# Performance work log

Measured on AMD Instinct MI355X. Metric: run time of the kernel, lower is better.

Reference implementation:

```python
import jax, jax.numpy as jnp
import numpy as np

DIM, HEADS, WS = 256, 16, 8
B, H, W = 2, 252, 252
BN_EPS = 1e-5


def _rel_index():
    # Same construction as the torch buffer relative_position_index (64,64)
    coords = np.stack(np.meshgrid(np.arange(WS), np.arange(WS), indexing='ij'))
    flat = coords.reshape(2, -1)
    rel = (flat[:, :, None] - flat[:, None, :]).transpose(1, 2, 0).copy()
    rel[..., 0] += WS - 1
    rel[..., 1] += WS - 1
    rel[..., 0] *= 2 * WS - 1
    return jnp.asarray(rel.sum(-1))

REL_IDX = _rel_index()  # (WS*WS, WS*WS) int


def _conv(x, w, pad, groups=1):
    return jax.lax.conv_general_dilated(
        x, w, (1, 1), [(pad[0], pad[0]), (pad[1], pad[1])],
        dimension_numbers=('NCHW', 'OIHW', 'NCHW'), feature_group_count=groups)


def setup_inputs() -> dict:
    key = jax.random.key(0)
    ks = jax.random.split(key, 8)
    s = lambda k, shape, sc: jax.random.normal(k, shape, jnp.float32) * sc
    z = lambda: jnp.zeros((DIM,), jnp.float32)
    return {
        'x': s(ks[0], (B, DIM, H, W), 1.0),
        'w_qkv': s(ks[1], (3 * DIM, DIM, 1, 1), 0.05),
        'rel_bias_table': s(ks[2], ((2 * WS - 1) ** 2, HEADS), 0.02),
        'w_h': s(ks[3], (DIM, DIM, WS, 1), 0.02),
        'b_h': z(),
        'w_v': s(ks[4], (DIM, DIM, 1, WS), 0.02),
        'b_v': z(),
        'w_dw': s(ks[5], (DIM, 1, WS, WS), 0.05),
        'bn_gamma': jnp.ones((DIM,), jnp.float32),
        'bn_beta': z(),
        'bn_mean': z(),
        'bn_var': jnp.ones((DIM,), jnp.float32),
        'w_pw': s(ks[6], (DIM, DIM, 1, 1), 0.05),
    }


def reference(x, w_qkv, rel_bias_table, w_h, b_h, w_v, b_v, w_dw,
              bn_gamma, bn_beta, bn_mean, bn_var, w_pw):
    Bc, C, Hc, Wc = x.shape
    pad_h, pad_w = WS - Hc % WS, WS - Wc % WS
    xp = jnp.pad(x, ((0, 0), (0, 0), (0, pad_h), (0, pad_w)), mode='reflect')
    Hp, Wp = Hc + pad_h, Wc + pad_w
    hh, ww, d = Hp // WS, Wp // WS, C // HEADS

    qkv = _conv(xp, w_qkv, (0, 0))  # (B, 3C, Hp, Wp)
    # b (qkv h d) (hh ws1) (ww ws2) -> qkv (b hh ww) h (ws1 ws2) d
    qkv = qkv.reshape(Bc, 3, HEADS, d, hh, WS, ww, WS)
    qkv = qkv.transpose(1, 0, 4, 6, 2, 5, 7, 3).reshape(3, Bc * hh * ww, HEADS, WS * WS, d)
    q, k, v = qkv[0], qkv[1], qkv[2]

    dots = jnp.einsum('nhid,nhjd->nhij', q, k) * (d ** -0.5)
    bias = rel_bias_table[REL_IDX.reshape(-1)].reshape(WS * WS, WS * WS, HEADS)
    dots = dots + bias.transpose(2, 0, 1)[None]  # (1, h, 64, 64)
    attn = jax.nn.softmax(dots, axis=-1)
    out = jnp.einsum('nhij,nhjd->nhid', attn, v)
    # (b hh ww) h (ws1 ws2) d -> b (h d) (hh ws1) (ww ws2)
    out = out.reshape(Bc, hh, ww, HEADS, WS, WS, d)
    out = out.transpose(0, 3, 6, 1, 4, 2, 5).reshape(Bc, C, Hp, Wp)
    out = out[:, :, :Hc, :Wc]

    p1 = _conv(jnp.pad(out, ((0, 0), (0, 0), (0, 1), (0, 0)), mode='reflect'),
               w_h, (WS // 2 - 1, 0)) + b_h[None, :, None, None]
    p2 = _conv(jnp.pad(out, ((0, 0), (0, 0), (0, 0), (0, 1)), mode='reflect'),
               w_v, (0, WS // 2 - 1)) + b_v[None, :, None, None]
    y = jnp.pad(p1 + p2, ((0, 0), (0, 0), (0, 1), (0, 1)), mode='reflect')
    y = _conv(y, w_dw, ((WS - 1) // 2, (WS - 1) // 2), groups=DIM)  # depthwise
    inv = bn_gamma / jnp.sqrt(bn_var + BN_EPS)
    y = y * inv[None, :, None, None] + (bn_beta - bn_mean * inv)[None, :, None, None]
    y = _conv(y, w_pw, (0, 0))  # pointwise 1x1
    return y[:, :, :Hc, :Wc]
```

## Files before the change

kernel.cpp:

```cpp
#include <hip/hip_runtime.h>
#include <hip/hip_bf16.h>

#define HC 252
#define WC 252
#define CD 256
#define NHEADS 16

#define XP_W 264
#define XP_ROW (XP_W*256)
#define XP_BH  (252*XP_ROW)

typedef unsigned short u16;
typedef unsigned int u32;
typedef __attribute__((ext_vector_type(8))) short bf16x8;
typedef __attribute__((ext_vector_type(4))) float f32x4;
typedef __attribute__((ext_vector_type(4))) u32 u32x4;
typedef __attribute__((ext_vector_type(2))) u32 u32x2;

#define XP_BYTES (2u * 2u * (unsigned)XP_BH)
#define ZP_OFF   XP_BYTES
#define ZP_BYTES 409600u
#define WT_OFF   (ZP_OFF + ZP_BYTES)
#define WT_ELEMS (128*8192)
#define WPW_OFF  (WT_OFF + (unsigned)WT_ELEMS*2u)
#define WPW_ELEMS (8*8192)
#define WQ_OFF   (WPW_OFF + (unsigned)WPW_ELEMS*2u)
#define WQ_ELEMS (768*256)
#define BIAS_OFF (WQ_OFF + (unsigned)WQ_ELEMS*2u)
#define HALO_ZERO_ELEMS (2*252*11*256)

__device__ __forceinline__ u16 bfu(float f) {
    __hip_bfloat16 h = __float2bfloat16(f);
    return *(reinterpret_cast<u16*>(&h));
}
__device__ __forceinline__ u32 pack2(float a, float b) {
    return (u32)bfu(a) | ((u32)bfu(b) << 16);
}
__device__ __forceinline__ float bf2f(u16 v) {
    union { u32 u; float f; } cv; cv.u = ((u32)v) << 16; return cv.f;
}

__global__ __launch_bounds__(256, 2) void attn_mfma(
    const float* __restrict__ x, const u16* __restrict__ WQ,
    const float* __restrict__ BIASF, u16* __restrict__ xp)
{
    __shared__ __align__(16) char smem[57344];

    const int bid = blockIdx.x;
    const int zz = (bid & 7) * 256 + (bid >> 3);
    const int wx = zz & 31, wy = (zz >> 5) & 31, b = zz >> 10;
    const int tid = threadIdx.x;
    const int lane = tid & 63, wid = tid >> 6;
    const int g = lane >> 4, li = lane & 15;

    {
        int ci = tid;
        const float* srcc = x + (size_t)(b * 256 + ci) * (HC * WC);
        #pragma unroll
        for (int r = 0; r < 8; ++r) {
            int h = wy * 8 + r; if (h >= HC) h = 2 * HC - 2 - h;
            const float* src = srcc + h * WC;
            float v[8];
            if (wx == 31) {
                #pragma unroll
                for (int c = 0; c < 8; ++c) {
                    int w = 248 + c; if (w >= WC) w = 2 * WC - 2 - w;
                    v[c] = src[w];
                }
            } else {
                float4 f0 = *(const float4*)(src + wx * 8);
                float4 f1 = *(const float4*)(src + wx * 8 + 4);
                v[0]=f0.x; v[1]=f0.y; v[2]=f0.z; v[3]=f0.w;
                v[4]=f1.x; v[5]=f1.y; v[6]=f1.z; v[7]=f1.w;
            }
            #pragma unroll
            for (int c = 0; c < 8; ++c) {
                int pos = r * 8 + c;
                int byte = pos * 512 + ((ci * 2) ^ ((pos & 7) << 4));
                *(u16*)(smem + byte) = bfu(v[c]);
            }
        }
    }
    __syncthreads();

    const int WB = 32768 + wid * 6144;
    char* Vb = smem + WB;
    char* Pb = smem + WB + 2048;

    const bf16x8 zf = {0,0,0,0,0,0,0,0};

    #pragma unroll 1
    for (int hh = 0; hh < 4; ++hh) {
        const int head = wid * 4 + hh;

        f32x4 acc[3][4];
        #pragma unroll
        for (int p = 0; p < 3; ++p)
            #pragma unroll
            for (int nf = 0; nf < 4; ++nf) acc[p][nf] = (f32x4){0.f,0.f,0.f,0.f};

        for (int ks = 0; ks < 8; ++ks) {
            bf16x8 bx[4];
            #pragma unroll
            for (int nf = 0; nf < 4; ++nf) {
                int pos = 16 * nf + li;
                int byte = pos * 512 + ((ks * 64 + 16 * g) ^ ((pos & 7) << 4));
                bx[nf] = *(const bf16x8*)(smem + byte);
            }
            bf16x8 aw[3];
            #pragma unroll
            for (int p = 0; p < 3; ++p) {
                int o = p * 256 + head * 16 + li;
                aw[p] = *(const bf16x8*)(WQ + o * 256 + ks * 32 + 8 * g);
            }
            __builtin_amdgcn_s_setprio(1);
            #pragma unroll
            for (int p = 0; p < 3; ++p)
                #pragma unroll
                for (int nf = 0; nf < 4; ++nf)
                    acc[p][nf] = __builtin_amdgcn_mfma_f32_16x16x32_bf16(aw[p], bx[nf], acc[p][nf], 0, 0, 0);
            __builtin_amdgcn_s_setprio(0);
        }

        bf16x8 qf[4], kf[4];
        const int sA = 32 * g + li;
        #pragma unroll
        for (int nf = 0; nf < 4; ++nf) {
            #pragma unroll
            for (int p = 0; p < 2; ++p) {
                u32 w0 = pack2(acc[p][nf][0], acc[p][nf][1]);
                u32 w1 = pack2(acc[p][nf][2], acc[p][nf][3]);
                union { bf16x8 v; u32 u[4]; } f;
                f.u[0] = (u32)__shfl((int)w0, sA);
                f.u[1] = (u32)__shfl((int)w1, sA);
                f.u[2] = (u32)__shfl((int)w0, sA + 16);
                f.u[3] = (u32)__shfl((int)w1, sA + 16);
                bf16x8 fv = (g < 2) ? f.v : zf;
                if (p == 0) qf[nf] = fv; else kf[nf] = fv;
            }
        }

        #pragma unroll
        for (int nf = 0; nf < 4; ++nf) {
            int pos = 16 * nf + li;
            #pragma unroll
            for (int r = 0; r < 4; ++r) {
                int d = 4 * g + r;
                int byte = (pos >> 3) * 256 + d * 16 + (pos & 7) * 2;
                *(u16*)(Vb + byte) = bfu(acc[2][nf][r]);
            }
        }

        f32x4 s[4][4];
        #pragma unroll
        for (int mf = 0; mf < 4; ++mf)
            #pragma unroll
            for (int nf = 0; nf < 4; ++nf) s[mf][nf] = (f32x4){0.f,0.f,0.f,0.f};
        __builtin_amdgcn_s_setprio(1);
        #pragma unroll
        for (int mf = 0; mf < 4; ++mf)
            #pragma unroll
            for (int nf = 0; nf < 4; ++nf)
                s[mf][nf] = __builtin_amdgcn_mfma_f32_16x16x32_bf16(qf[mf], kf[nf], s[mf][nf], 0, 0, 0);
        __builtin_amdgcn_s_setprio(0);

        f32x4 e[4][4];
        f32x4 rs[4];
        #pragma unroll
        for (int mf = 0; mf < 4; ++mf) rs[mf] = (f32x4){0.f,0.f,0.f,0.f};
        #pragma unroll
        for (int mf = 0; mf < 4; ++mf)
            #pragma unroll
            for (int nf = 0; nf < 4; ++nf) {
                f32x4 b4 = *(const f32x4*)(BIASF + (((head * 4 + mf) * 4 + nf) * 64 + lane) * 4);
                #pragma unroll
                for (int r = 0; r < 4; ++r) {
                    float ev = __expf(s[mf][nf][r] * 0.25f + b4[r]);
                    e[mf][nf][r] = ev;
                    rs[mf][r] += ev;
                }
            }
        #pragma unroll
        for (int mf = 0; mf < 4; ++mf)
            #pragma unroll
            for (int r = 0; r < 4; ++r) {
                float t = rs[mf][r];
                t += __shfl_xor(t, 1); t += __shfl_xor(t, 2);
                t += __shfl_xor(t, 4); t += __shfl_xor(t, 8);
                rs[mf][r] = t;
            }

        f32x4 o[4];
        #pragma unroll
        for (int mf = 0; mf < 4; ++mf) o[mf] = (f32x4){0.f,0.f,0.f,0.f};
        const bool even = !(lane & 1);
        #pragma unroll
        for (int hf = 0; hf < 2; ++hf) {
            #pragma unroll
            for (int mf = 0; mf < 4; ++mf)
                #pragma unroll
                for (int nfl = 0; nfl < 2; ++nfl) {
                    f32x4 ee = e[mf][2 * hf + nfl];
                    float p0 = __shfl_xor(ee[0], 1), p1 = __shfl_xor(ee[1], 1);
                    float p2 = __shfl_xor(ee[2], 1), p3 = __shfl_xor(ee[3], 1);
                    int jl = 16 * nfl + (li & ~1);
                    u32 w0, w1; int r0;
                    if (even) { w0 = pack2(ee[0], p0); w1 = pack2(ee[1], p1); r0 = 0; }
                    else      { w0 = pack2(p2, ee[2]); w1 = pack2(p3, ee[3]); r0 = 2; }
                    int i0 = 16 * mf + 4 * g + r0, i1 = i0 + 1;
                    *(u32*)(Pb + i0 * 64 + ((2 * jl) ^ ((i0 & 3) << 4))) = w0;
                    *(u32*)(Pb + i1 * 64 + ((2 * jl) ^ ((i1 & 3) << 4))) = w1;
                }
            bf16x8 bv = *(const bf16x8*)(Vb + (4 * hf + g) * 256 + li * 16);
            __builtin_amdgcn_s_setprio(1);
            #pragma unroll
            for (int mf = 0; mf < 4; ++mf) {
                int i = 16 * mf + li;
                bf16x8 ap = *(const bf16x8*)(Pb + i * 64 + ((16 * g) ^ ((i & 3) << 4)));
                o[mf] = __builtin_amdgcn_mfma_f32_16x16x32_bf16(ap, bv, o[mf], 0, 0, 0);
            }
            __builtin_amdgcn_s_setprio(0);
        }

        #pragma unroll
        for (int mf = 0; mf < 4; ++mf) {
            int h = wy * 8 + 2 * mf + (g >> 1);
            int wbase = wx * 8 + 4 * (g & 1);
            if (h < HC && wbase < WC) {
                size_t rowb = ((size_t)(b * HC + h)) * XP_ROW + (size_t)(head * 16 + li);
                #pragma unroll
                for (int r = 0; r < 4; ++r) {
                    float v = o[mf][r] / rs[mf][r];
                    u16 bv = bfu(v);
                    xp[rowb + (size_t)(wbase + r + 4) * 256] = bv;
                    if (wbase + r == 250) xp[rowb + (size_t)256 * 256] = bv;
                }
            }
        }
    }
}

__global__ __launch_bounds__(256) void wprep_kernel(
    const float* __restrict__ wh, const float* __restrict__ wv,
    const float* __restrict__ wpw, const float* __restrict__ wqkv,
    const float* __restrict__ btab, u16* __restrict__ wsu)
{
    int i = blockIdx.x * 256 + threadIdx.x;
    u16* WT = wsu + WT_OFF / 2;
    u16* WP = wsu + WPW_OFF / 2;
    u16* ZP = wsu + ZP_OFF / 2;
    u16* WQp = wsu + WQ_OFF / 2;
    float* BF = (float*)(wsu + BIAS_OFF / 2);
    if (i < WT_ELEMS) {
        int j = i & 7, l = (i >> 3) & 1023, s = i >> 13;
        int kb = (l >> 8) & 3;
        int co = (l & 255) ^ (kb << 1);
        float v;
        if (s < 64) {
            int t = s >> 3, ci = (s & 7) * 32 + kb * 8 + j;
            v = wh[co * 2048 + ci * 8 + t];
        } else {
            int s2 = s - 64;
            int t = s2 >> 3, ci = (s2 & 7) * 32 + kb * 8 + j;
            v = wv[co * 2048 + ci * 8 + t];
        }
        WT[i] = bfu(v);
    } else if (i < WT_ELEMS + WPW_ELEMS) {
        int i2 = i - WT_ELEMS;
        int j = i2 & 7, l = (i2 >> 3) & 1023, s = i2 >> 13;
        int kb = (l >> 8) & 3;
        int co = (l & 255) ^ (kb << 1);
        WP[i2] = bfu(wpw[co * 256 + s * 32 + kb * 8 + j]);
    } else if (i < WT_ELEMS + WPW_ELEMS + (int)(ZP_BYTES / 2)) {
        ZP[i - WT_ELEMS - WPW_ELEMS] = 0;
    } else if (i < WT_ELEMS + WPW_ELEMS + (int)(ZP_BYTES / 2) + WQ_ELEMS) {
        int i4 = i - WT_ELEMS - WPW_ELEMS - (int)(ZP_BYTES / 2);
        WQp[i4] = bfu(wqkv[i4]);
    } else {
        int i5 = i - WT_ELEMS - WPW_ELEMS - (int)(ZP_BYTES / 2) - WQ_ELEMS;
        if (i5 < 16384) {
            int lane = i5 & 63, nf = (i5 >> 6) & 3, mf = (i5 >> 8) & 3, head = i5 >> 10;
            int gg = lane >> 4, ll = lane & 15;
            #pragma unroll
            for (int r = 0; r < 4; ++r) {
                int row = 16 * mf + 4 * gg + r;
                int col = 16 * nf + ll;
                int dy = (row >> 3) - (col >> 3) + 7;
                int dx = (row & 7) - (col & 7) + 7;
                BF[i5 * 4 + r] = btab[(dy * 15 + dx) * NHEADS + head];
            }
        } else {
            int i6 = i5 - 16384;
            if (i6 < HALO_ZERO_ELEMS) {
                int ci = i6 & 255;
                int c11 = (i6 >> 8) % 11;
                int row = i6 / (11 * 256);
                int wp = (c11 < 4) ? c11 : 253 + c11;
                wsu[(size_t)row * XP_ROW + (size_t)wp * 256 + ci] = 0;
            }
        }
    }
}

__global__ __launch_bounds__(512, 2) void sepconv_mfma(
    const u16* __restrict__ xpt, const u16* __restrict__ WT,
    const u16* __restrict__ ZP,
    const float* __restrict__ b_h, const float* __restrict__ b_v,
    u16* __restrict__ P)
{
    __shared__ __align__(16) u16 Bs[2][256 * 36];

    const int bid = blockIdx.x;
    const int zz = (bid & 7) * 63 + (bid >> 3);
    const int h = zz % HC, b = zz / HC;
    const int tid = threadIdx.x;
    const int lane = tid & 63, wid = tid >> 6;
    const int wr = wid >> 2, wc = wid & 3;
    const int cq = lane & 15, kb = lane >> 4;

    const int wB = tid & 255;
    const int oc0 = tid >> 8;
    const int tb = (wB + 4) * 256 + oc0 * 8;
    const int bsw = wB * 36 + oc0 * 8;

    const int afb = (kb * 256 + wr * 128 + (cq ^ (kb << 1))) * 8;

    const u16* const xb = xpt + (size_t)(b * HC) * XP_ROW;

    f32x4 acc[8][4];
    #pragma unroll
    for (int m = 0; m < 8; ++m)
        #pragma unroll
        for (int n = 0; n < 4; ++n) acc[m][n] = (f32x4){0.f, 0.f, 0.f, 0.f};

    u32x4 rB0, rB1;

#define SC_SRC(t, RP, SO)                                                      \
    if ((t) < 64) {                                                            \
        int tt = (t) >> 3;                                                     \
        int jt = h + tt - 3;                                                   \
        int jr = (jt == 252) ? 250 : jt;                                       \
        RP = (jt >= 0 && jt <= 252) ? (xpt + ((size_t)(b * HC) + jr) * XP_ROW) : ZP; \
        SO = ((t) & 7) * 32;                                                   \
    } else {                                                                   \
        int tt = ((t) - 64) >> 3;                                              \
        RP = xb + (size_t)h * XP_ROW + (tt - 3) * 256;                         \
        SO = (((t) - 64) & 7) * 32;                                            \
    }

    {
        const u16* rp; int so;
        SC_SRC(0, rp, so)
        rB0 = *(const u32x4*)(rp + so + tb);
        rB1 = *(const u32x4*)(rp + so + tb + 16);
    }
    *(u32x4*)&Bs[0][bsw] = rB0;
    *(u32x4*)&Bs[0][bsw + 16] = rB1;

    #pragma unroll 1
    for (int s = 0; s < 128; ++s) {
        const int cur = s & 1;
        const int s1 = s + 1;
        __syncthreads();

        const u16* wts = WT + (size_t)s * 8192 + afb;
        bf16x8 af[8];
        #pragma unroll
        for (int m = 0; m < 8; ++m)
            af[m] = *(const bf16x8*)(wts + m * 128);

        if (s1 < 128) {
            const u16* rp; int so;
            SC_SRC(s1, rp, so)
            rB0 = *(const u32x4*)(rp + so + tb);
            rB1 = *(const u32x4*)(rp + so + tb + 16);
        }

        {
            bf16x8 bfr[4];
            #pragma unroll
            for (int n = 0; n < 4; ++n)
                bfr[n] = *(const bf16x8*)&Bs[cur][(wc * 64 + n * 16 + cq) * 36 + kb * 8];
            __builtin_amdgcn_s_setprio(1);
            #pragma unroll
            for (int m = 0; m < 8; ++m)
                #pragma unroll
                for (int n = 0; n < 4; ++n)
                    acc[m][n] = __builtin_amdgcn_mfma_f32_16x16x32_bf16(af[m], bfr[n], acc[m][n], 0, 0, 0);
            __builtin_amdgcn_s_setprio(0);
        }

        if (s1 < 128) {
            const int nxt = cur ^ 1;
            *(u32x4*)&Bs[nxt][bsw] = rB0;
            *(u32x4*)&Bs[nxt][bsw + 16] = rB1;
        }
    }
#undef SC_SRC

    const int rq = lane >> 4, cc = lane & 15;
    #pragma unroll
    for (int m = 0; m < 8; ++m) {
        int cgb = wr * 128 + m * 16 + rq * 4;
        float bias[4];
        #pragma unroll
        for (int rr = 0; rr < 4; ++rr) bias[rr] = b_h[cgb + rr] + b_v[cgb + rr];
        #pragma unroll
        for (int n = 0; n < 4; ++n) {
            int wg = wc * 64 + n * 16 + cc;
            if (wg < WC) {
                #pragma unroll
                for (int rr = 0; rr < 4; ++rr)
                    P[((size_t)(b * CD + cgb + rr) * HC + h) * WC + wg] = bfu(acc[m][n][rr] + bias[rr]);
            }
        }
    }
}

__global__ __launch_bounds__(256) void dwbn_kernel(
    const u16* __restrict__ P, const float* __restrict__ w_dw,
    const float* __restrict__ gamma, const float* __restrict__ beta,
    const float* __restrict__ mean, const float* __restrict__ var,
    __hip_bfloat16* __restrict__ Yb)
{
    __shared__ float ps[23][73];
    __shared__ float wd[64];
    const int bw = blockIdx.x, bh = blockIdx.y, bz = blockIdx.z;
    const int b = bz >> 8, c = bz & 255;
    const int h0 = bh * 16, w0 = bw * 64;
    const int tid = threadIdx.x;
    if (tid < 64) wd[tid] = w_dw[c * 64 + tid];
    for (int it = 0; it < 7; ++it) {
        int flat = tid + it * 256;
        if (flat < 23 * 71) {
            int row = flat / 71, col = flat % 71;
            int j = h0 - 3 + row, wcol = w0 - 3 + col;
            float v = 0.f;
            if (j >= 0 && j <= HC && wcol >= 0 && wcol <= WC) {
                int jr = (j == HC) ? (HC - 2) : j;
                int wr2 = (wcol == WC) ? (WC - 2) : wcol;
                v = bf2f(P[((size_t)(b * CD + c) * HC + jr) * WC + wr2]);
            }
            ps[row][col] = v;
        }
    }
    __syncthreads();
    const int r = tid >> 4;
    const int c0 = (tid & 15) * 4;
    const int h = h0 + r, w = w0 + c0;
    if (h < HC && w < WC) {
        float s0 = 0.f, s1 = 0.f, s2 = 0.f, s3 = 0.f;
        #pragma unroll
        for (int u = 0; u < 8; ++u)
            #pragma unroll
            for (int v2 = 0; v2 < 8; ++v2) {
                const float wv = wd[u * 8 + v2];
                const float* pr = &ps[r + u][c0 + v2];
                s0 += wv * pr[0]; s1 += wv * pr[1];
                s2 += wv * pr[2]; s3 += wv * pr[3];
            }
        const float inv = gamma[c] * rsqrtf(var[c] + 1e-5f);
        const float sh = beta[c] - mean[c] * inv;
        u32x2 pk;
        pk[0] = pack2(s0 * inv + sh, s1 * inv + sh);
        pk[1] = pack2(s2 * inv + sh, s3 * inv + sh);
        *(u32x2*)&Yb[((size_t)(b * CD + c) * HC + h) * WC + w] = pk;
    }
}

__global__ __launch_bounds__(512, 2) void pw_mfma(
    const u16* __restrict__ Y, const u16* __restrict__ WP,
    float* __restrict__ O)
{
    __shared__ __align__(16) u16 As[2][8192];
    __shared__ __align__(16) u16 Bs[2][256 * 36];

    const int bid = blockIdx.x;
    const int zz = (bid & 7) * 63 + (bid >> 3);
    const int h = zz % HC, b = zz / HC;
    const int tid = threadIdx.x;
    const int lane = tid & 63, wid = tid >> 6;
    const int wr = wid >> 2, wc = wid & 3;
    const int cq = lane & 15, kb = lane >> 4;

    const int wl2 = (tid & 127) * 2;
    const int oc = tid >> 7;

    const u16* yb = Y + ((size_t)(b * 256 + oc * 8) * HC + h) * WC + wl2;

    const int bw0 = wl2 * 36 + oc * 8;
    const int bw1 = bw0 + 36;

    f32x4 acc[8][4];
    #pragma unroll
    for (int m = 0; m < 8; ++m)
        #pragma unroll
        for (int n = 0; n < 4; ++n) acc[m][n] = (f32x4){0.f, 0.f, 0.f, 0.f};

    u32x4 rA[2];
    u32 rB[8];

    rA[0] = *(const u32x4*)(WP + (size_t)tid * 8);
    rA[1] = *(const u32x4*)(WP + (size_t)(512 + tid) * 8);
    #pragma unroll
    for (int j = 0; j < 8; ++j)
        rB[j] = *(const u32*)(yb + (size_t)j * (HC * WC));
    *(u32x4*)&As[0][(size_t)tid * 8] = rA[0];
    *(u32x4*)&As[0][(size_t)(512 + tid) * 8] = rA[1];
    {
        union { bf16x8 v; u32 u[4]; } p0, p1;
        #pragma unroll
        for (int q = 0; q < 4; ++q) {
            p0.u[q] = __builtin_amdgcn_perm(rB[2 * q + 1], rB[2 * q], 0x05040100u);
            p1.u[q] = __builtin_amdgcn_perm(rB[2 * q + 1], rB[2 * q], 0x07060302u);
        }
        *(bf16x8*)&Bs[0][bw0] = p0.v;
        *(bf16x8*)&Bs[0][bw1] = p1.v;
    }

    #pragma unroll 1
    for (int s = 0; s < 8; ++s) {
        const int cur = s & 1;
        const int s1 = s + 1;
        if (s1 < 8) {
            rA[0] = *(const u32x4*)(WP + (size_t)s1 * 8192 + (size_t)tid * 8);
            rA[1] = *(const u32x4*)(WP + (size_t)s1 * 8192 + (size_t)(512 + tid) * 8);
            #pragma unroll
            for (int j = 0; j < 8; ++j)
                rB[j] = *(const u32*)(yb + (size_t)(s1 * 32 + j) * (HC * WC));
        }
        __syncthreads();

        {
            bf16x8 af[8], bfr[4];
            #pragma unroll
            for (int m = 0; m < 8; ++m) {
                int row = wr * 128 + m * 16 + cq;
                af[m] = *(const bf16x8*)&As[cur][(kb * 256 + (row ^ (kb << 1))) * 8];
            }
            #pragma unroll
            for (int n = 0; n < 4; ++n)
                bfr[n] = *(const bf16x8*)&Bs[cur][(wc * 64 + n * 16 + cq) * 36 + kb * 8];
            __builtin_amdgcn_s_setprio(1);
            #pragma unroll
            for (int m = 0; m < 8; ++m)
                #pragma unroll
                for (int n = 0; n < 4; ++n)
                    acc[m][n] = __builtin_amdgcn_mfma_f32_16x16x32_bf16(af[m], bfr[n], acc[m][n], 0, 0, 0);
            __builtin_amdgcn_s_setprio(0);
        }

        if (s1 < 8) {
            const int nxt = cur ^ 1;
            *(u32x4*)&As[nxt][(size_t)tid * 8] = rA[0];
            *(u32x4*)&As[nxt][(size_t)(512 + tid) * 8] = rA[1];
            union { bf16x8 v; u32 u[4]; } p0, p1;
            #pragma unroll
            for (int q = 0; q < 4; ++q) {
                p0.u[q] = __builtin_amdgcn_perm(rB[2 * q + 1], rB[2 * q], 0x05040100u);
                p1.u[q] = __builtin_amdgcn_perm(rB[2 * q + 1], rB[2 * q], 0x07060302u);
            }
            *(bf16x8*)&Bs[nxt][bw0] = p0.v;
            *(bf16x8*)&Bs[nxt][bw1] = p1.v;
        }
    }

    __syncthreads();
    float* tsl = (float*)&Bs[0][0] + wid * (16 * 68);
    const int rq = lane >> 4;
    const int r2 = lane >> 2;
    const int wq = (lane & 3) * 16;
    #pragma unroll
    for (int m = 0; m < 8; ++m) {
        #pragma unroll
        for (int n = 0; n < 4; ++n)
            #pragma unroll
            for (int rr = 0; rr < 4; ++rr)
                tsl[(rq * 4 + rr) * 68 + n * 16 + cq] = acc[m][n][rr];
        const int co = wr * 128 + m * 16 + r2;
        float* orow = O + ((size_t)(b * CD + co) * HC + h) * WC + wc * 64;
        #pragma unroll
        for (int q = 0; q < 4; ++q) {
            int wl = wq + 4 * q;
            if (wc * 64 + wl < WC) {
                f32x4 v4 = *(const f32x4*)&tsl[r2 * 68 + wl];
                *(f32x4*)&orow[wl] = v4;
            }
        }
    }
}

extern "C" void kernel_launch(void* const* d_in, const int* in_sizes, int n_in,
                              void* d_out, int out_size, void* d_ws, size_t ws_size,
                              hipStream_t stream)
{
    const float* x      = (const float*)d_in[0];
    const float* w_qkv  = (const float*)d_in[1];
    const float* bias_t = (const float*)d_in[2];
    const float* w_h    = (const float*)d_in[3];
    const float* b_h    = (const float*)d_in[4];
    const float* w_v    = (const float*)d_in[5];
    const float* b_v    = (const float*)d_in[6];
    const float* w_dw   = (const float*)d_in[7];
    const float* bn_g   = (const float*)d_in[8];
    const float* bn_b   = (const float*)d_in[9];
    const float* bn_m   = (const float*)d_in[10];
    const float* bn_v   = (const float*)d_in[11];
    const float* w_pw   = (const float*)d_in[12];
    float* out = (float*)d_out;

    u16* wsu = (u16*)d_ws;
    const u16* XPu = wsu;
    const u16* ZPu = wsu + ZP_OFF / 2;
    const u16* WTu = wsu + WT_OFF / 2;
    const u16* WPu = wsu + WPW_OFF / 2;
    const u16* WQu = wsu + WQ_OFF / 2;
    const float* BFu = (const float*)(wsu + BIAS_OFF / 2);

    wprep_kernel<<<11529, 256, 0, stream>>>(w_h, w_v, w_pw, w_qkv, bias_t, wsu);
    attn_mfma<<<2048, 256, 0, stream>>>(x, WQu, BFu, wsu);
    sepconv_mfma<<<504, 512, 0, stream>>>(XPu, WTu, ZPu, b_h, b_v, (u16*)d_out);
    dwbn_kernel<<<dim3(4, 16, 512), 256, 0, stream>>>((const u16*)d_out, w_dw, bn_g, bn_b,
                                                      bn_m, bn_v, (__hip_bfloat16*)d_ws);
    pw_mfma<<<504, 512, 0, stream>>>(wsu, WPu, out);
}
```

Before: 762.0 us.

## Split sepconv GEMM into 128x128 tiles and stage weights through LDS

The separable-conv MFMA kernel now uses 256-thread blocks, each computing a 128-output-channel by 128-column tile, giving 2016 blocks instead of 504 blocks that covered the full 256x256 row. Weight fragments no longer go straight from global memory into registers. They are double-buffered through LDS with an XOR swizzle, and the global loads are issued before the barrier. The aim is better occupancy, lower register pressure and better latency hiding. In exchange, each input row slab and each weight slice is loaded by more blocks, and every step now writes weights to LDS.

```diff
diff --git a/kernel.cpp b/kernel.cpp
--- a/kernel.cpp
+++ b/kernel.cpp
@@ -302,37 +302,43 @@
     }
 }
 
-__global__ __launch_bounds__(512, 2) void sepconv_mfma(
+__global__ __launch_bounds__(256) void sepconv_mfma(
     const u16* __restrict__ xpt, const u16* __restrict__ WT,
     const u16* __restrict__ ZP,
     const float* __restrict__ b_h, const float* __restrict__ b_v,
     u16* __restrict__ P)
 {
-    __shared__ __align__(16) u16 Bs[2][256 * 36];
+    __shared__ __align__(16) u16 As[2][4096];
+    __shared__ __align__(16) u16 Bs[2][128 * 36];
 
     const int bid = blockIdx.x;
-    const int zz = (bid & 7) * 63 + (bid >> 3);
-    const int h = zz % HC, b = zz / HC;
+    const int zz = (bid & 7) * 252 + (bid >> 3);
+    const int bh = zz >> 2, q = zz & 3;
+    const int ct = q >> 1, wt = q & 1;
+    const int h = bh % HC, b = bh / HC;
+    const int co0 = ct * 128, w0 = wt * 128;
     const int tid = threadIdx.x;
     const int lane = tid & 63, wid = tid >> 6;
-    const int wr = wid >> 2, wc = wid & 3;
+    const int wr = wid >> 1, wc = wid & 1;
     const int cq = lane & 15, kb = lane >> 4;
 
-    const int wB = tid & 255;
-    const int oc0 = tid >> 8;
-    const int tb = (wB + 4) * 256 + oc0 * 8;
+    const int wB = tid & 127;
+    const int oc0 = tid >> 7;
+    const int tb = (w0 + wB + 4) * 256 + oc0 * 8;
     const int bsw = wB * 36 + oc0 * 8;
 
-    const int afb = (kb * 256 + wr * 128 + (cq ^ (kb << 1))) * 8;
+    const int a0 = ((tid >> 7) * 256 + co0 + (tid & 127)) * 8;
+    const int a1 = (((tid >> 7) + 2) * 256 + co0 + (tid & 127)) * 8;
 
     const u16* const xb = xpt + (size_t)(b * HC) * XP_ROW;
 
-    f32x4 acc[8][4];
+    f32x4 acc[4][4];
     #pragma unroll
-    for (int m = 0; m < 8; ++m)
+    for (int m = 0; m < 4; ++m)
         #pragma unroll
         for (int n = 0; n < 4; ++n) acc[m][n] = (f32x4){0.f, 0.f, 0.f, 0.f};
 
+    u32x4 rA[2];
     u32x4 rB0, rB1;
 
 #define SC_SRC(t, RP, SO)                                                      \
@@ -348,12 +354,16 @@
         SO = (((t) - 64) & 7) * 32;                                            \
     }
 
+    rA[0] = *(const u32x4*)(WT + a0);
+    rA[1] = *(const u32x4*)(WT + a1);
     {
         const u16* rp; int so;
         SC_SRC(0, rp, so)
         rB0 = *(const u32x4*)(rp + so + tb);
         rB1 = *(const u32x4*)(rp + so + tb + 16);
     }
+    *(u32x4*)&As[0][(size_t)tid * 8] = rA[0];
+    *(u32x4*)&As[0][(size_t)(256 + tid) * 8] = rA[1];
     *(u32x4*)&Bs[0][bsw] = rB0;
     *(u32x4*)&Bs[0][bsw + 16] = rB1;
 
@@ -361,29 +371,29 @@
     for (int s = 0; s < 128; ++s) {
         const int cur = s & 1;
         const int s1 = s + 1;
-        __syncthreads();
-
-        const u16* wts = WT + (size_t)s * 8192 + afb;
-        bf16x8 af[8];
-        #pragma unroll
-        for (int m = 0; m < 8; ++m)
-            af[m] = *(const bf16x8*)(wts + m * 128);
-
         if (s1 < 128) {
+            rA[0] = *(const u32x4*)(WT + (size_t)s1 * 8192 + a0);
+            rA[1] = *(const u32x4*)(WT + (size_t)s1 * 8192 + a1);
             const u16* rp; int so;
             SC_SRC(s1, rp, so)
             rB0 = *(const u32x4*)(rp + so + tb);
             rB1 = *(const u32x4*)(rp + so + tb + 16);
         }
+        __syncthreads();
 
         {
-            bf16x8 bfr[4];
+            bf16x8 af[4], bfr[4];
+            #pragma unroll
+            for (int m = 0; m < 4; ++m) {
+                int row = wr * 64 + m * 16 + cq;
+                af[m] = *(const bf16x8*)&As[cur][(kb * 128 + (row ^ (kb << 1))) * 8];
+            }
             #pragma unroll
             for (int n = 0; n < 4; ++n)
                 bfr[n] = *(const bf16x8*)&Bs[cur][(wc * 64 + n * 16 + cq) * 36 + kb * 8];
             __builtin_amdgcn_s_setprio(1);
             #pragma unroll
-            for (int m = 0; m < 8; ++m)
+            for (int m = 0; m < 4; ++m)
                 #pragma unroll
                 for (int n = 0; n < 4; ++n)
                     acc[m][n] = __builtin_amdgcn_mfma_f32_16x16x32_bf16(af[m], bfr[n], acc[m][n], 0, 0, 0);
@@ -392,6 +402,8 @@
 
         if (s1 < 128) {
             const int nxt = cur ^ 1;
+            *(u32x4*)&As[nxt][(size_t)tid * 8] = rA[0];
+            *(u32x4*)&As[nxt][(size_t)(256 + tid) * 8] = rA[1];
             *(u32x4*)&Bs[nxt][bsw] = rB0;
             *(u32x4*)&Bs[nxt][bsw + 16] = rB1;
         }
@@ -400,14 +412,14 @@
 
     const int rq = lane >> 4, cc = lane & 15;
     #pragma unroll
-    for (int m = 0; m < 8; ++m) {
-        int cgb = wr * 128 + m * 16 + rq * 4;
+    for (int m = 0; m < 4; ++m) {
+        int cgb = co0 + wr * 64 + m * 16 + rq * 4;
         float bias[4];
         #pragma unroll
         for (int rr = 0; rr < 4; ++rr) bias[rr] = b_h[cgb + rr] + b_v[cgb + rr];
         #pragma unroll
         for (int n = 0; n < 4; ++n) {
-            int wg = wc * 64 + n * 16 + cc;
+            int wg = w0 + wc * 64 + n * 16 + cc;
             if (wg < WC) {
                 #pragma unroll
                 for (int rr = 0; rr < 4; ++rr)
@@ -619,7 +631,7 @@
 
     wprep_kernel<<<11529, 256, 0, stream>>>(w_h, w_v, w_pw, w_qkv, bias_t, wsu);
     attn_mfma<<<2048, 256, 0, stream>>>(x, WQu, BFu, wsu);
-    sepconv_mfma<<<504, 512, 0, stream>>>(XPu, WTu, ZPu, b_h, b_v, (u16*)d_out);
+    sepconv_mfma<<<2016, 256, 0, stream>>>(XPu, WTu, ZPu, b_h, b_v, (u16*)d_out);
     dwbn_kernel<<<dim3(4, 16, 512), 256, 0, stream>>>((const u16*)d_out, w_dw, bn_g, bn_b,
                                                       bn_m, bn_v, (__hip_bfloat16*)d_ws);
     pw_mfma<<<504, 512, 0, stream>>>(wsu, WPu, out);
```

Measured after the change: 690.8 us. -9.3%, faster.
